# Performance work log

Measured on AMD Instinct MI355X. Metric: run time of the kernel, lower is better.

Reference implementation:

```python
import jax, jax.numpy as jnp
import numpy as np

B, S, H, E, V, T = 512, 140, 512, 256, 1000, 21  # T = day_walk_max + 1
PAD, SOS = 0, 2
NDAYS, DLEN = 7, 20


def setup_inputs() -> dict:
    key = jax.random.key(0)
    ks = jax.random.split(key, 16)
    s = 0.05
    return {
        "encoder_hidden": jax.random.normal(ks[0], (1, B, H), jnp.float32),
        "encoder_outputs": jax.random.normal(ks[1], (B, S, H), jnp.float32),
        "label": jax.random.randint(ks[2], (B, T + 1), 0, V),
        "numpairs": jax.random.randint(ks[3], (B, S), 0, 10),
        "emb": jax.random.normal(ks[4], (V, E), jnp.float32) * s,
        "W_ih": jax.random.normal(ks[5], (3 * H, E), jnp.float32) * s,
        "W_hh": jax.random.normal(ks[6], (3 * H, H), jnp.float32) * s,
        "b_ih": jnp.zeros((3 * H,), jnp.float32),
        "b_hh": jnp.zeros((3 * H,), jnp.float32),
        "attn_Wa": jax.random.normal(ks[7], (H, H), jnp.float32) * s,
        "wa_W": jax.random.normal(ks[8], (H, 2 * H), jnp.float32) * s,
        "fc_W": jax.random.normal(ks[9], (V, H), jnp.float32) * s,
        "fc_b": jnp.zeros((V,), jnp.float32),
    }


def _decode(encoder_hidden, encoder_outputs, label, numpairs,
            emb, W_ih, W_hh, b_ih, b_hh, attn_Wa, wa_W, fc_W, fc_b):
    # Luong 'general' attention over 7 day-segments of 20 steps each.
    enc_days = encoder_outputs.reshape(B, NDAYS, DLEN, H)
    mask_day = numpairs.reshape(B, NDAYS, DLEN) != PAD
    # energy is hidden-independent: precompute once  [B,7,20,H]
    energy_day = jnp.einsum('bdsh,gh->bdsg', enc_days, attn_Wa)

    def step(carry, lab_t):
        dec_in, h = carry  # dec_in [B] int, h [B,H]
        # per-day additive attention with numpair padding mask
        sc = jnp.einsum('bh,bdsh->bds', h, energy_day)
        sc = jnp.where(mask_day, sc, jnp.float32(-1e9))
        wd = jax.nn.softmax(sc, axis=-1)
        week = jnp.einsum('bds,bdsh->bdh', wd, enc_days)  # [B,7,H]
        # GRU cell (PyTorch gate layout r,z,n); dropout is identity at eval
        x = emb[dec_in]  # [B,E]
        gi = x @ W_ih.T + b_ih
        gh = h @ W_hh.T + b_hh
        i_r, i_z, i_n = jnp.split(gi, 3, axis=-1)
        h_r, h_z, h_n = jnp.split(gh, 3, axis=-1)
        r = jax.nn.sigmoid(i_r + h_r)
        z = jax.nn.sigmoid(i_z + h_z)
        n = jnp.tanh(i_n + r * h_n)
        h_new = (1.0 - z) * n + z * h  # [B,H]
        # week-level attention over the 7 day contexts (no mask)
        ew = jnp.einsum('bdh,gh->bdg', week, attn_Wa)
        aw = jax.nn.softmax(jnp.einsum('bh,bdh->bd', h_new, ew), axis=-1)
        ctx = jnp.einsum('bd,bdh->bh', aw, week)
        concat = jnp.concatenate([h_new, ctx], axis=-1)  # [B,2H]
        out = jax.nn.log_softmax(jnp.tanh(concat @ wa_W.T) @ fc_W.T + fc_b, axis=-1)
        return (lab_t, h_new), out  # teacher forcing: next input = label[:, t]

    dec0 = jnp.full((B,), SOS, dtype=label.dtype)
    h0 = encoder_hidden[0]  # [B,H]
    labels_t = label[:, :T].T  # [T,B]
    (last_in, _), outs = jax.lax.scan(step, (dec0, h0), labels_t)
    decoder_outputs = jnp.transpose(outs, (1, 0, 2))  # [B,T,V]
    return decoder_outputs, last_in[:, None]


def reference(encoder_hidden, encoder_outputs, label, numpairs,
              emb, W_ih, W_hh, b_ih, b_hh, attn_Wa, wa_W, fc_W, fc_b):
    return _decode(encoder_hidden, encoder_outputs, label, numpairs,
                   emb, W_ih, W_hh, b_ih, b_hh, attn_Wa, wa_W, fc_W, fc_b)
```

## Files before the change

### kernel.cpp

```cpp
#include <hip/hip_runtime.h>
#include <math.h>

typedef __attribute__((ext_vector_type(8))) short bf16x8;
typedef __attribute__((ext_vector_type(4))) float f32x4;

constexpr int NB = 512;
constexpr int NS = 140;
constexpr int NH = 512;
constexpr int NE = 256;
constexpr int NV = 1000;
constexpr int NVP = 1024;
constexpr int NT = 21;
constexpr int ND = 7;
constexpr int DL = 20;
constexpr int SOS = 2;
constexpr int LSTR = NT + 1;
constexpr int NROW = NT * NB;

__device__ __forceinline__ unsigned short f2bf(float f) {
  union { float f; unsigned u; } v; v.f = f;
  unsigned r = v.u + 0x7fffu + ((v.u >> 16) & 1u);
  return (unsigned short)(r >> 16);
}
__device__ __forceinline__ float bf2f(unsigned short h) {
  union { unsigned u; float f; } v; v.u = ((unsigned)h) << 16;
  return v.f;
}
__device__ __forceinline__ void unp8(uint4 v, float* o) {
  o[0] = bf2f((unsigned short)(v.x & 0xffffu)); o[1] = bf2f((unsigned short)(v.x >> 16));
  o[2] = bf2f((unsigned short)(v.y & 0xffffu)); o[3] = bf2f((unsigned short)(v.y >> 16));
  o[4] = bf2f((unsigned short)(v.z & 0xffffu)); o[5] = bf2f((unsigned short)(v.z >> 16));
  o[6] = bf2f((unsigned short)(v.w & 0xffffu)); o[7] = bf2f((unsigned short)(v.w >> 16));
}

template<int A16, int EPI, int OUT16>
__device__ __forceinline__ void gemm_body(
    const float* __restrict__ Af, const unsigned short* __restrict__ Ah,
    const unsigned short* __restrict__ Bt, const float* __restrict__ bias,
    float* __restrict__ C, unsigned short* __restrict__ C16,
    int K, int lda, int ldc, int bx, int by,
    unsigned short* As, unsigned short* Bs)
{
  const int tid = threadIdx.x;
  const int rowBase = by * 64, colBase = bx * 64;
  const int wave = tid >> 6, lane = tid & 63, quad = lane >> 4, l15 = lane & 15;
  const int rw = (wave & 1) * 32, cw = (wave >> 1) * 32;

  f32x4 acc[2][2];
#pragma unroll
  for (int i = 0; i < 2; ++i)
#pragma unroll
    for (int j = 0; j < 2; ++j)
#pragma unroll
      for (int r = 0; r < 4; ++r) acc[i][j][r] = 0.f;

  const int ar = tid >> 2;
  const int kq = (tid & 3) * 8;
  const float* aptrf = nullptr;
  const unsigned short* aptrh = nullptr;
  if (A16) aptrh = Ah + (size_t)(rowBase + ar) * lda + kq;
  else     aptrf = Af + (size_t)(rowBase + ar) * lda + kq;
  const unsigned short* bptr = Bt + (size_t)(colBase + ar) * K + kq;
  unsigned short* asd = &As[ar * 40 + kq];
  unsigned short* bsd = &Bs[ar * 40 + kq];

  float4 x0, x1;
  uint4 av;
  if (A16) {
    av = *(const uint4*)aptrh;
  } else {
    x0 = *(const float4*)aptrf; x1 = *(const float4*)(aptrf + 4);
  }
  uint4 bv = *(const uint4*)bptr;

  int cur = 0;
  for (int k0 = 0; k0 < K; k0 += 32) {
    uint4 aw;
    if (A16) {
      aw = av;
    } else {
      aw.x = (unsigned)f2bf(x0.x) | ((unsigned)f2bf(x0.y) << 16);
      aw.y = (unsigned)f2bf(x0.z) | ((unsigned)f2bf(x0.w) << 16);
      aw.z = (unsigned)f2bf(x1.x) | ((unsigned)f2bf(x1.y) << 16);
      aw.w = (unsigned)f2bf(x1.z) | ((unsigned)f2bf(x1.w) << 16);
    }
    *(uint4*)(asd + cur * 2560) = aw;
    *(uint4*)(bsd + cur * 2560) = bv;

    const int kn = k0 + 32;
    if (kn < K) {
      if (A16) {
        av = *(const uint4*)(aptrh + kn);
      } else {
        x0 = *(const float4*)(aptrf + kn);
        x1 = *(const float4*)(aptrf + kn + 4);
      }
      bv = *(const uint4*)(bptr + kn);
    }
    __syncthreads();

    const unsigned short* Ab = As + cur * 2560;
    const unsigned short* Bb = Bs + cur * 2560;
    const bf16x8 af0 = *(const bf16x8*)&Ab[(rw + l15) * 40 + quad * 8];
    const bf16x8 af1 = *(const bf16x8*)&Ab[(rw + 16 + l15) * 40 + quad * 8];
    const bf16x8 bf0 = *(const bf16x8*)&Bb[(cw + l15) * 40 + quad * 8];
    const bf16x8 bf1 = *(const bf16x8*)&Bb[(cw + 16 + l15) * 40 + quad * 8];
    acc[0][0] = __builtin_amdgcn_mfma_f32_16x16x32_bf16(af0, bf0, acc[0][0], 0, 0, 0);
    acc[0][1] = __builtin_amdgcn_mfma_f32_16x16x32_bf16(af0, bf1, acc[0][1], 0, 0, 0);
    acc[1][0] = __builtin_amdgcn_mfma_f32_16x16x32_bf16(af1, bf0, acc[1][0], 0, 0, 0);
    acc[1][1] = __builtin_amdgcn_mfma_f32_16x16x32_bf16(af1, bf1, acc[1][1], 0, 0, 0);
    cur ^= 1;
  }

#pragma unroll
  for (int i = 0; i < 2; ++i) {
    const int grow = rowBase + rw + 16 * i + quad * 4;
#pragma unroll
    for (int j = 0; j < 2; ++j) {
      const int gcol = colBase + cw + 16 * j + l15;
#pragma unroll
      for (int r = 0; r < 4; ++r) {
        float vo = acc[i][j][r];
        if (EPI == 1) vo += (gcol < NV) ? bias[gcol] : 0.f;
        if (EPI == 2) vo = tanhf(vo);
        if (OUT16) C16[(size_t)(grow + r) * ldc + gcol] = f2bf(vo);
        else       C[(size_t)(grow + r) * ldc + gcol] = vo;
      }
    }
  }
}

template<int A16, int EPI, int OUT16>
__global__ __launch_bounds__(256) void gemm_k(
    const float* __restrict__ Af, const unsigned short* __restrict__ Ah,
    const unsigned short* __restrict__ Bt, const float* __restrict__ bias,
    float* __restrict__ C, unsigned short* __restrict__ C16,
    int K, int lda, int ldc)
{
  __shared__ unsigned short As[2 * 64 * 40];
  __shared__ unsigned short Bs[2 * 64 * 40];
  gemm_body<A16, EPI, OUT16>(Af, Ah, Bt, bias, C, C16, K, lda, ldc,
                             blockIdx.x, blockIdx.y, As, Bs);
}

__global__ __launch_bounds__(256) void gemm_gather(
    const float* __restrict__ emb, const unsigned short* __restrict__ Wiht,
    unsigned short* __restrict__ Gi, const int* __restrict__ label)
{
  __shared__ unsigned short As[64 * 40];
  __shared__ unsigned short Bs[64 * 40];
  const int tid = threadIdx.x;
  const int rowBase = blockIdx.y * 64, colBase = blockIdx.x * 64;
  const int wave = tid >> 6, lane = tid & 63, quad = lane >> 4, l15 = lane & 15;
  const int rw = (wave & 1) * 32, cw = (wave >> 1) * 32;
  const int K = 256;

  f32x4 acc[2][2];
#pragma unroll
  for (int i = 0; i < 2; ++i)
#pragma unroll
    for (int j = 0; j < 2; ++j)
#pragma unroll
      for (int r = 0; r < 4; ++r) acc[i][j][r] = 0.f;

  const int ar = tid >> 2;
  const int kq = (tid & 3) * 8;
  const int aRowG = rowBase + ar;
  const int t = aRowG >> 9;
  const int b = aRowG & 511;
  const int dec = (t == 0) ? SOS : label[b * LSTR + (t - 1)];
  const float* aptr = emb + (size_t)dec * NE + kq;
  const unsigned short* bptr = Wiht + (size_t)(colBase + ar) * K + kq;
  unsigned short* asd = &As[ar * 40 + kq];
  unsigned short* bsd = &Bs[ar * 40 + kq];

  float4 x0 = *(const float4*)aptr;
  float4 x1 = *(const float4*)(aptr + 4);
  uint4 bv = *(const uint4*)bptr;

  for (int k0 = 0; k0 < K; k0 += 32) {
    uint4 aw;
    aw.x = (unsigned)f2bf(x0.x) | ((unsigned)f2bf(x0.y) << 16);
    aw.y = (unsigned)f2bf(x0.z) | ((unsigned)f2bf(x0.w) << 16);
    aw.z = (unsigned)f2bf(x1.x) | ((unsigned)f2bf(x1.y) << 16);
    aw.w = (unsigned)f2bf(x1.z) | ((unsigned)f2bf(x1.w) << 16);
    *(uint4*)asd = aw;
    *(uint4*)bsd = bv;
    __syncthreads();
    const int kn = k0 + 32;
    if (kn < K) {
      x0 = *(const float4*)(aptr + kn);
      x1 = *(const float4*)(aptr + kn + 4);
      bv = *(const uint4*)(bptr + kn);
    }
    const bf16x8 af0 = *(const bf16x8*)&As[(rw + l15) * 40 + quad * 8];
    const bf16x8 af1 = *(const bf16x8*)&As[(rw + 16 + l15) * 40 + quad * 8];
    const bf16x8 bf0 = *(const bf16x8*)&Bs[(cw + l15) * 40 + quad * 8];
    const bf16x8 bf1 = *(const bf16x8*)&Bs[(cw + 16 + l15) * 40 + quad * 8];
    acc[0][0] = __builtin_amdgcn_mfma_f32_16x16x32_bf16(af0, bf0, acc[0][0], 0, 0, 0);
    acc[0][1] = __builtin_amdgcn_mfma_f32_16x16x32_bf16(af0, bf1, acc[0][1], 0, 0, 0);
    acc[1][0] = __builtin_amdgcn_mfma_f32_16x16x32_bf16(af1, bf0, acc[1][0], 0, 0, 0);
    acc[1][1] = __builtin_amdgcn_mfma_f32_16x16x32_bf16(af1, bf1, acc[1][1], 0, 0, 0);
    __syncthreads();
  }

#pragma unroll
  for (int i = 0; i < 2; ++i) {
    const int grow = rowBase + rw + 16 * i + quad * 4;
#pragma unroll
    for (int j = 0; j < 2; ++j) {
      const int gcol = colBase + cw + 16 * j + l15;
#pragma unroll
      for (int r = 0; r < 4; ++r)
        Gi[(size_t)(grow + r) * 1536 + gcol] = f2bf(acc[i][j][r]);
    }
  }
}

__global__ __launch_bounds__(256) void step_fused(
    const float* __restrict__ Ht, const unsigned short* __restrict__ W1pk,
    const unsigned short* __restrict__ Gi_t,
    const float* __restrict__ b_ih, const float* __restrict__ b_hh,
    float* __restrict__ Hnext, float* __restrict__ Ut, int notLast)
{
  __shared__ __align__(16) char smem[46080];
  unsigned short* As = (unsigned short*)smem;
  unsigned short* Bs = (unsigned short*)(smem + 5120);
  float* Gbuf = (float*)smem;

  const int tid = threadIdx.x;
  const int wave = tid >> 6, lane = tid & 63, quad = lane >> 4, l15 = lane & 15;
  const int rowBase = blockIdx.y * 32;
  const int colBase = blockIdx.x * 256;

  f32x4 acc[2][4];
#pragma unroll
  for (int i = 0; i < 2; ++i)
#pragma unroll
    for (int j = 0; j < 4; ++j)
#pragma unroll
      for (int r = 0; r < 4; ++r) acc[i][j][r] = 0.f;

  const int ar = tid >> 3;
  const int kqa = (tid & 7) * 4;
  const float* aptr = Ht + (size_t)(rowBase + ar) * NH + kqa;
  const unsigned short* bbase = W1pk + (size_t)(colBase + tid) * 32;
  unsigned short* asd = As + ar * 40 + kqa;
  unsigned short* bsd = Bs + tid * 40;

  float4 xa = *(const float4*)aptr;
  uint4 bv0 = *(const uint4*)(bbase + 0);
  uint4 bv1 = *(const uint4*)(bbase + 8);
  uint4 bv2 = *(const uint4*)(bbase + 16);
  uint4 bv3 = *(const uint4*)(bbase + 24);

  int cur = 0;
  for (int k0 = 0; k0 < NH; k0 += 32) {
    ushort4 aw;
    aw.x = f2bf(xa.x); aw.y = f2bf(xa.y); aw.z = f2bf(xa.z); aw.w = f2bf(xa.w);
    *(ushort4*)(asd + cur * 1280) = aw;
    *(uint4*)(bsd + cur * 10240 + 0)  = bv0;
    *(uint4*)(bsd + cur * 10240 + 8)  = bv1;
    *(uint4*)(bsd + cur * 10240 + 16) = bv2;
    *(uint4*)(bsd + cur * 10240 + 24) = bv3;

    const int kn = k0 + 32;
    if (kn < NH) {
      xa = *(const float4*)(aptr + kn);
      const unsigned short* nb = bbase + (size_t)(kn >> 5) * (2048 * 32);
      bv0 = *(const uint4*)(nb + 0);
      bv1 = *(const uint4*)(nb + 8);
      bv2 = *(const uint4*)(nb + 16);
      bv3 = *(const uint4*)(nb + 24);
    }
    __syncthreads();

    const unsigned short* Ab = As + cur * 1280;
    const unsigned short* Bb = Bs + cur * 10240;
    const bf16x8 af0 = *(const bf16x8*)&Ab[(l15) * 40 + quad * 8];
    const bf16x8 af1 = *(const bf16x8*)&Ab[(16 + l15) * 40 + quad * 8];
#pragma unroll
    for (int j = 0; j < 4; ++j) {
      const bf16x8 bf = *(const bf16x8*)&Bb[(wave * 64 + j * 16 + l15) * 40 + quad * 8];
      acc[0][j] = __builtin_amdgcn_mfma_f32_16x16x32_bf16(af0, bf, acc[0][j], 0, 0, 0);
      acc[1][j] = __builtin_amdgcn_mfma_f32_16x16x32_bf16(af1, bf, acc[1][j], 0, 0, 0);
    }
    cur ^= 1;
  }
  __syncthreads();

#pragma unroll
  for (int i = 0; i < 2; ++i) {
#pragma unroll
    for (int j = 0; j < 4; ++j) {
#pragma unroll
      for (int r = 0; r < 4; ++r) {
        const int rl = 16 * i + quad * 4 + r;
        const int col = j * 16 + l15;
        if (wave == 3)
          Ut[(size_t)(rowBase + rl) * NH + blockIdx.x * 64 + col] = acc[i][j][r];
        else
          Gbuf[(wave * 32 + rl) * 72 + col] = acc[i][j][r];
      }
    }
  }
  __syncthreads();

  if (notLast) {
    const int rl = tid >> 3, c8 = (tid & 7) * 8;
    const int bg = rowBase + rl;
    const int jg = blockIdx.x * 64 + c8;
    const float* g0 = Gbuf + (0 * 32 + rl) * 72 + c8;
    const float* g1 = Gbuf + (1 * 32 + rl) * 72 + c8;
    const float* g2 = Gbuf + (2 * 32 + rl) * 72 + c8;
    const unsigned short* gp = Gi_t + (size_t)bg * 1536;
    float gr[8], gz[8], gn[8];
    { uint4 a = *(const uint4*)(gp + jg);        unp8(a, gr); }
    { uint4 a = *(const uint4*)(gp + 512 + jg);  unp8(a, gz); }
    { uint4 a = *(const uint4*)(gp + 1024 + jg); unp8(a, gn); }
    const float* hR = Ht + (size_t)bg * NH + jg;
    float* hW = Hnext + (size_t)bg * NH + jg;
    const float4 ho0 = *(const float4*)hR;
    const float4 ho1 = *(const float4*)(hR + 4);
    const float hov[8] = {ho0.x, ho0.y, ho0.z, ho0.w, ho1.x, ho1.y, ho1.z, ho1.w};
    float o[8];
#pragma unroll
    for (int c = 0; c < 8; ++c) {
      const int j = jg + c;
      const float ir  = gr[c] + b_ih[j];
      const float iz  = gz[c] + b_ih[512 + j];
      const float inn = gn[c] + b_ih[1024 + j];
      const float hr  = g0[c] + b_hh[j];
      const float hz  = g1[c] + b_hh[512 + j];
      const float hn  = g2[c] + b_hh[1024 + j];
      const float rg = 1.f / (1.f + expf(-(ir + hr)));
      const float zg = 1.f / (1.f + expf(-(iz + hz)));
      const float ng = tanhf(inn + rg * hn);
      o[c] = (1.f - zg) * ng + zg * hov[c];
    }
    *(float4*)hW = make_float4(o[0], o[1], o[2], o[3]);
    *(float4*)(hW + 4) = make_float4(o[4], o[5], o[6], o[7]);
  }
}

__global__ __launch_bounds__(256) void day_attn_mfma(
    const float* __restrict__ enc, const int* __restrict__ numpairs,
    const float* __restrict__ U, unsigned short* __restrict__ week)
{
  __shared__ unsigned short Erow[32 * 520];
  __shared__ unsigned short ETs[512 * 40];
  __shared__ float S_lds[32 * 33];
  __shared__ unsigned short P_lds[32 * 40];

  const int tid = threadIdx.x;
  const int wave = tid >> 6, lane = tid & 63;
  const int quad = lane >> 4, l15 = lane & 15;
  const int b = blockIdx.x / ND, d = blockIdx.x % ND;
  const int mt = wave >> 1, nt = wave & 1;

  {
    unsigned* p2 = (unsigned*)ETs;
    for (int i = tid; i < 10240; i += 256) p2[i] = 0;
    unsigned* p3 = (unsigned*)P_lds;
    for (int i = tid; i < 640; i += 256) p3[i] = 0;
  }

  const float* eb = enc + ((size_t)b * NS + d * DL) * NH;
  for (int f = tid; f < DL * NH / 4; f += 256) {
    const int s = f >> 7, c4 = f & 127, h = c4 * 4;
    const float4 v = *(const float4*)(eb + s * NH + h);
    const unsigned short h0 = f2bf(v.x), h1 = f2bf(v.y),
                         h2 = f2bf(v.z), h3 = f2bf(v.w);
    ushort4 hs; hs.x = h0; hs.y = h1; hs.z = h2; hs.w = h3;
    *(ushort4*)&Erow[s * 520 + h] = hs;
    ETs[(h + 0) * 40 + s] = h0;
    ETs[(h + 1) * 40 + s] = h1;
    ETs[(h + 2) * 40 + s] = h2;
    ETs[(h + 3) * 40 + s] = h3;
  }

  bf16x8 qa[16];
  {
    const int m = mt * 16 + l15;
    const int t = (m < NT + 1) ? m : NT;
    const float* qp = U + ((size_t)t * NB + b) * NH + quad * 8;
#pragma unroll
    for (int ks = 0; ks < 16; ++ks) {
      const float4 lo = *(const float4*)(qp + ks * 32);
      const float4 hi = *(const float4*)(qp + ks * 32 + 4);
      union { bf16x8 v; ushort u[8]; } pk;
      pk.u[0] = f2bf(lo.x); pk.u[1] = f2bf(lo.y); pk.u[2] = f2bf(lo.z); pk.u[3] = f2bf(lo.w);
      pk.u[4] = f2bf(hi.x); pk.u[5] = f2bf(hi.y); pk.u[6] = f2bf(hi.z); pk.u[7] = f2bf(hi.w);
      qa[ks] = pk.v;
    }
  }
  __syncthreads();

  f32x4 sacc = {0.f, 0.f, 0.f, 0.f};
#pragma unroll
  for (int ks = 0; ks < 16; ++ks) {
    const bf16x8 bf = *(const bf16x8*)&Erow[(nt * 16 + l15) * 520 + ks * 32 + quad * 8];
    sacc = __builtin_amdgcn_mfma_f32_16x16x32_bf16(qa[ks], bf, sacc, 0, 0, 0);
  }
#pragma unroll
  for (int r = 0; r < 4; ++r)
    S_lds[(mt * 16 + quad * 4 + r) * 33 + nt * 16 + l15] = sacc[r];
  __syncthreads();

  {
    const int r = tid >> 3, c = tid & 7;
    const int base = b * NS + d * DL;
    float v0 = S_lds[r * 33 + c];
    if (numpairs[base + c] == 0) v0 = -1e9f;
    float v1 = S_lds[r * 33 + c + 8];
    if (numpairs[base + c + 8] == 0) v1 = -1e9f;
    float v2 = -1e30f;
    if (c < 4) {
      v2 = S_lds[r * 33 + c + 16];
      if (numpairs[base + c + 16] == 0) v2 = -1e9f;
    }
    float mx = fmaxf(fmaxf(v0, v1), v2);
    mx = fmaxf(mx, __shfl_xor(mx, 1));
    mx = fmaxf(mx, __shfl_xor(mx, 2));
    mx = fmaxf(mx, __shfl_xor(mx, 4));
    const float e0 = expf(v0 - mx), e1 = expf(v1 - mx);
    const float e2 = (c < 4) ? expf(v2 - mx) : 0.f;
    float sm = e0 + e1 + e2;
    sm += __shfl_xor(sm, 1);
    sm += __shfl_xor(sm, 2);
    sm += __shfl_xor(sm, 4);
    const float inv = 1.f / sm;
    P_lds[r * 40 + c] = f2bf(e0 * inv);
    P_lds[r * 40 + c + 8] = f2bf(e1 * inv);
    if (c < 4) P_lds[r * 40 + c + 16] = f2bf(e2 * inv);
  }
  __syncthreads();

  const bf16x8 pa = *(const bf16x8*)&P_lds[(mt * 16 + l15) * 40 + quad * 8];
#pragma unroll
  for (int j = 0; j < 16; ++j) {
    const int hcol = nt * 256 + j * 16;
    const bf16x8 bf = *(const bf16x8*)&ETs[(hcol + l15) * 40 + quad * 8];
    f32x4 oacc = {0.f, 0.f, 0.f, 0.f};
    oacc = __builtin_amdgcn_mfma_f32_16x16x32_bf16(pa, bf, oacc, 0, 0, 0);
#pragma unroll
    for (int r = 0; r < 4; ++r) {
      const int t = mt * 16 + quad * 4 + r;
      if (t < NT)
        week[(((size_t)t * NB + b) * ND + d) * NH + hcol + l15] = f2bf(oacc[r]);
    }
  }
}

__global__ __launch_bounds__(256) void wk_ctx(
    const float* __restrict__ U, const unsigned short* __restrict__ week,
    const float* __restrict__ H, unsigned short* __restrict__ concat)
{
  __shared__ float scS[16 * ND];
  __shared__ float awS[16 * ND];
  const int tid = threadIdx.x;
  const int t = blockIdx.x >> 5;
  const int grp = blockIdx.x & 31;
  const int b16 = tid >> 4, k16 = tid & 15;
  const int b = grp * 16 + b16;
  const float* vp = U + ((size_t)(t + 1) * NB + b) * NH + k16 * 32;
  const size_t wrow = ((size_t)t * NB + b) * ND;

  for (int d = 0; d < ND; ++d) {
    const unsigned short* wp = week + (wrow + d) * NH + k16 * 32;
    float p = 0.f;
#pragma unroll
    for (int q = 0; q < 8; ++q) {
      const float4 a = *(const float4*)(vp + q * 4);
      const ushort4 wv = *(const ushort4*)(wp + q * 4);
      p += a.x * bf2f(wv.x) + a.y * bf2f(wv.y) + a.z * bf2f(wv.z) + a.w * bf2f(wv.w);
    }
    p += __shfl_down(p, 8); p += __shfl_down(p, 4);
    p += __shfl_down(p, 2); p += __shfl_down(p, 1);
    if (k16 == 0) scS[b16 * ND + d] = p;
  }
  __syncthreads();
  if (tid < 16) {
    float s[ND], mx = -1e30f;
    for (int d = 0; d < ND; ++d) { s[d] = scS[tid * ND + d]; mx = fmaxf(mx, s[d]); }
    float sum = 0.f;
    for (int d = 0; d < ND; ++d) { float e = expf(s[d] - mx); s[d] = e; sum += e; }
    const float inv = 1.f / sum;
    for (int d = 0; d < ND; ++d) awS[tid * ND + d] = s[d] * inv;
  }
  __syncthreads();

  const int c0 = k16 * 32;
  const float* hp = H + ((size_t)(t + 1) * NB + b) * NH + c0;
  float aw[ND];
#pragma unroll
  for (int d = 0; d < ND; ++d) aw[d] = awS[b16 * ND + d];
  unsigned short* crow = concat + ((size_t)t * NB + b) * 1024;
#pragma unroll
  for (int q = 0; q < 8; ++q) {
    const int c = c0 + q * 4;
    const float4 hv = *(const float4*)(hp + q * 4);
    ushort4 hs;
    hs.x = f2bf(hv.x); hs.y = f2bf(hv.y); hs.z = f2bf(hv.z); hs.w = f2bf(hv.w);
    *(ushort4*)(crow + c) = hs;
    float4 cv = make_float4(0.f, 0.f, 0.f, 0.f);
#pragma unroll
    for (int d = 0; d < ND; ++d) {
      const ushort4 wv = *(const ushort4*)(week + (wrow + d) * NH + c);
      cv.x += aw[d] * bf2f(wv.x); cv.y += aw[d] * bf2f(wv.y);
      cv.z += aw[d] * bf2f(wv.z); cv.w += aw[d] * bf2f(wv.w);
    }
    ushort4 cs;
    cs.x = f2bf(cv.x); cs.y = f2bf(cv.y); cs.z = f2bf(cv.z); cs.w = f2bf(cv.w);
    *(ushort4*)(crow + 512 + c) = cs;
  }
}

__global__ __launch_bounds__(256) void lsm_k(
    const float* __restrict__ logits, float* __restrict__ out)
{
  __shared__ float red[8];
  const int tid = threadIdx.x;
  const int wave = tid >> 6, lane = tid & 63;
  const int r = blockIdx.x;
  const int t = r >> 9, b = r & (NB - 1);
  const float* row = logits + (size_t)r * NVP;
  float v[4];
  float mx = -1e30f;
#pragma unroll
  for (int k = 0; k < 4; ++k) {
    const int c = tid + k * 256;
    v[k] = row[c];
    if (c < NV) mx = fmaxf(mx, v[k]);
  }
#pragma unroll
  for (int off = 32; off; off >>= 1) mx = fmaxf(mx, __shfl_xor(mx, off));
  if (lane == 0) red[wave] = mx;
  __syncthreads();
  mx = fmaxf(fmaxf(red[0], red[1]), fmaxf(red[2], red[3]));
  float s = 0.f;
#pragma unroll
  for (int k = 0; k < 4; ++k) {
    const int c = tid + k * 256;
    if (c < NV) s += expf(v[k] - mx);
  }
#pragma unroll
  for (int off = 32; off; off >>= 1) s += __shfl_xor(s, off);
  if (lane == 0) red[4 + wave] = s;
  __syncthreads();
  const float lse = mx + logf(red[4] + red[5] + red[6] + red[7]);
  float* orow = out + ((size_t)b * NT + t) * NV;
#pragma unroll
  for (int k = 0; k < 4; ++k) {
    const int c = tid + k * 256;
    if (c < NV) orow[c] = v[k] - lse;
  }
}

__global__ void write_last(const int* __restrict__ label, float* __restrict__ out2)
{
  const int b = blockIdx.x * 256 + threadIdx.x;
  if (b < NB) out2[b] = (float)label[b * LSTR + (NT - 1)];
}

__global__ __launch_bounds__(256) void pack_w1pk(
    const float* __restrict__ Whh, const float* __restrict__ Wa,
    unsigned short* __restrict__ W1pk)
{
  const int idx = blockIdx.x * 256 + threadIdx.x;
  const int np = idx >> 9, k = idx & 511;
  const int g = np >> 8, rem = np & 255, gate = rem >> 6, j = g * 64 + (rem & 63);
  float v;
  if (gate < 3) v = Whh[(size_t)(gate * 512 + j) * 512 + k];
  else          v = Wa[(size_t)k * 512 + j];
  W1pk[((size_t)(k >> 5) * 2048 + np) * 32 + (k & 31)] = f2bf(v);
}

__global__ __launch_bounds__(256) void cast4(
    const float4* __restrict__ in, ushort4* __restrict__ out, int n4)
{
  const int i = blockIdx.x * 256 + threadIdx.x;
  if (i < n4) {
    const float4 x = in[i];
    ushort4 r;
    r.x = f2bf(x.x); r.y = f2bf(x.y); r.z = f2bf(x.z); r.w = f2bf(x.w);
    out[i] = r;
  }
}

extern "C" void kernel_launch(void* const* d_in, const int* in_sizes, int n_in,
                              void* d_out, int out_size, void* d_ws, size_t ws_size,
                              hipStream_t stream)
{
  const float* enc_h  = (const float*)d_in[0];
  const float* enc    = (const float*)d_in[1];
  const int*   label  = (const int*)d_in[2];
  const int*   numprs = (const int*)d_in[3];
  const float* emb    = (const float*)d_in[4];
  const float* W_ih   = (const float*)d_in[5];
  const float* W_hh   = (const float*)d_in[6];
  const float* b_ih   = (const float*)d_in[7];
  const float* b_hh   = (const float*)d_in[8];
  const float* Wa     = (const float*)d_in[9];
  const float* wa_W   = (const float*)d_in[10];
  const float* fc_W   = (const float*)d_in[11];
  const float* fc_b   = (const float*)d_in[12];
  float* out = (float*)d_out;

  float* f = (float*)d_ws;
  float* H_all   = f; f += (size_t)(NT + 1) * NB * NH;
  float* U_all   = f; f += (size_t)(NT + 1) * NB * NH;
  float* logitsW = f; f += (size_t)NROW * NVP;
  unsigned short* us = (unsigned short*)f;
  unsigned short* W1pk   = us; us += (size_t)2048 * 512;
  unsigned short* W3t    = us; us += (size_t)512 * 1024;
  unsigned short* W4t    = us; us += (size_t)NVP * 512;
  unsigned short* Wiht   = us; us += (size_t)1536 * 256;
  unsigned short* Gi     = us; us += (size_t)NT * NB * 1536;
  unsigned short* week   = us; us += (size_t)NT * NB * ND * NH;
  unsigned short* concatW= us; us += (size_t)NROW * 1024;
  unsigned short* aBuf   = us; us += (size_t)NROW * 512;

  const dim3 blk(256);
  const size_t BH = (size_t)NB * NH;

  hipMemcpyAsync(H_all, enc_h, BH * sizeof(float),
                 hipMemcpyDeviceToDevice, stream);

  pack_w1pk<<<dim3(2048 * 512 / 256), blk, 0, stream>>>(W_hh, Wa, W1pk);
  cast4<<<dim3(512 * 1024 / 4 / 256), blk, 0, stream>>>(
      (const float4*)wa_W, (ushort4*)W3t, 512 * 1024 / 4);
  cast4<<<dim3((NV * 512 / 4 + 255) / 256), blk, 0, stream>>>(
      (const float4*)fc_W, (ushort4*)W4t, NV * 512 / 4);
  hipMemsetAsync(W4t + (size_t)NV * 512, 0, (size_t)(NVP - NV) * 512 * 2, stream);
  cast4<<<dim3(1536 * 256 / 4 / 256), blk, 0, stream>>>(
      (const float4*)W_ih, (ushort4*)Wiht, 1536 * 256 / 4);
  gemm_gather<<<dim3(24, NT * 8), blk, 0, stream>>>(emb, Wiht, Gi, label);

  for (int t = 0; t <= NT; ++t) {
    const int notLast = (t < NT) ? 1 : 0;
    const int tg = (t < NT) ? t : NT - 1;
    step_fused<<<dim3(8, 16), blk, 0, stream>>>(
        H_all + (size_t)t * BH, W1pk, Gi + (size_t)tg * NB * 1536,
        b_ih, b_hh,
        H_all + (size_t)(notLast ? t + 1 : t) * BH,
        U_all + (size_t)t * BH, notLast);
  }

  day_attn_mfma<<<dim3(NB * ND), blk, 0, stream>>>(enc, numprs, U_all, week);
  wk_ctx<<<dim3(NT * 32), blk, 0, stream>>>(U_all, week, H_all, concatW);
  gemm_k<1, 2, 1><<<dim3(8, NROW / 64), blk, 0, stream>>>(
      nullptr, concatW, W3t, nullptr, nullptr, aBuf, 1024, 1024, 512);
  gemm_k<1, 1, 0><<<dim3(16, NROW / 64), blk, 0, stream>>>(
      nullptr, aBuf, W4t, fc_b, logitsW, nullptr, 512, 512, NVP);
  lsm_k<<<dim3(NROW), blk, 0, stream>>>(logitsW, out);
  write_last<<<dim3(2), blk, 0, stream>>>(label, out + (size_t)NB * NT * NV);
}
```

Baseline: 792.1 us.

## Run GRU recurrence as one cooperative persistent kernel and store U in bf16

Replaces the 22 per-step GRU kernel launches with a single cooperative kernel of 128 blocks that loops over time steps and uses grid.sync between steps, removing per-launch overhead and tail gaps. The K chunk grows from 32 to 64 (with W1pk repacked to match) so there are fewer LDS syncs per step. The attention projection U is written as bf16 instead of fp32, which halves its traffic and lets day_attn and wk_ctx load it without conversion. day_attn now builds its transposed encoder tile from LDS with a narrower stride and only zeroes the padding. The risks are grid-sync cost, the larger shared-memory footprint limiting co-residency, and the last step reading Gi at t=0 (its result is unused because notLast is 0).

```diff
diff --git a/kernel.cpp b/kernel.cpp
--- a/kernel.cpp
+++ b/kernel.cpp
@@ -1,5 +1,8 @@
 #include <hip/hip_runtime.h>
+#include <hip/hip_cooperative_groups.h>
 #include <math.h>
+
+namespace cg = cooperative_groups;
 
 typedef __attribute__((ext_vector_type(8))) short bf16x8;
 typedef __attribute__((ext_vector_type(4))) float f32x4;
@@ -217,138 +220,154 @@
   }
 }
 
-__global__ __launch_bounds__(256) void step_fused(
-    const float* __restrict__ Ht, const unsigned short* __restrict__ W1pk,
-    const unsigned short* __restrict__ Gi_t,
+__global__ __launch_bounds__(256) void gru_all(
+    float* __restrict__ H_all, const unsigned short* __restrict__ W1pk,
+    const unsigned short* __restrict__ Gi,
     const float* __restrict__ b_ih, const float* __restrict__ b_hh,
-    float* __restrict__ Hnext, float* __restrict__ Ut, int notLast)
-{
-  __shared__ __align__(16) char smem[46080];
+    unsigned short* __restrict__ U16)
+{
+  __shared__ __align__(16) char smem[82944];
   unsigned short* As = (unsigned short*)smem;
-  unsigned short* Bs = (unsigned short*)(smem + 5120);
+  unsigned short* Bs = (unsigned short*)(smem + 9216);
   float* Gbuf = (float*)smem;
 
   const int tid = threadIdx.x;
   const int wave = tid >> 6, lane = tid & 63, quad = lane >> 4, l15 = lane & 15;
   const int rowBase = blockIdx.y * 32;
   const int colBase = blockIdx.x * 256;
-
-  f32x4 acc[2][4];
-#pragma unroll
-  for (int i = 0; i < 2; ++i)
-#pragma unroll
-    for (int j = 0; j < 4; ++j)
-#pragma unroll
-      for (int r = 0; r < 4; ++r) acc[i][j][r] = 0.f;
-
-  const int ar = tid >> 3;
-  const int kqa = (tid & 7) * 4;
-  const float* aptr = Ht + (size_t)(rowBase + ar) * NH + kqa;
-  const unsigned short* bbase = W1pk + (size_t)(colBase + tid) * 32;
-  unsigned short* asd = As + ar * 40 + kqa;
-  unsigned short* bsd = Bs + tid * 40;
-
-  float4 xa = *(const float4*)aptr;
-  uint4 bv0 = *(const uint4*)(bbase + 0);
-  uint4 bv1 = *(const uint4*)(bbase + 8);
-  uint4 bv2 = *(const uint4*)(bbase + 16);
-  uint4 bv3 = *(const uint4*)(bbase + 24);
-
-  int cur = 0;
-  for (int k0 = 0; k0 < NH; k0 += 32) {
-    ushort4 aw;
-    aw.x = f2bf(xa.x); aw.y = f2bf(xa.y); aw.z = f2bf(xa.z); aw.w = f2bf(xa.w);
-    *(ushort4*)(asd + cur * 1280) = aw;
-    *(uint4*)(bsd + cur * 10240 + 0)  = bv0;
-    *(uint4*)(bsd + cur * 10240 + 8)  = bv1;
-    *(uint4*)(bsd + cur * 10240 + 16) = bv2;
-    *(uint4*)(bsd + cur * 10240 + 24) = bv3;
-
-    const int kn = k0 + 32;
-    if (kn < NH) {
-      xa = *(const float4*)(aptr + kn);
-      const unsigned short* nb = bbase + (size_t)(kn >> 5) * (2048 * 32);
-      bv0 = *(const uint4*)(nb + 0);
-      bv1 = *(const uint4*)(nb + 8);
-      bv2 = *(const uint4*)(nb + 16);
-      bv3 = *(const uint4*)(nb + 24);
+  const int arow = tid >> 3;
+  const int akq  = (tid & 7) * 8;
+  const size_t BH = (size_t)NB * NH;
+  cg::grid_group grid = cg::this_grid();
+
+  for (int t = 0; t <= NT; ++t) {
+    const float* Ht = H_all + (size_t)t * BH;
+    float* Hn = H_all + (size_t)(t + 1) * BH;
+    const unsigned short* Gt = Gi + (size_t)((t < NT) ? t : 0) * NB * 1536;
+    unsigned short* Ut = U16 + (size_t)t * BH;
+    const int notLast = (t < NT) ? 1 : 0;
+
+    f32x4 acc[2][4];
+#pragma unroll
+    for (int i = 0; i < 2; ++i)
+#pragma unroll
+      for (int j = 0; j < 4; ++j)
+#pragma unroll
+        for (int r = 0; r < 4; ++r) acc[i][j][r] = 0.f;
+
+    const float* aptr = Ht + (size_t)(rowBase + arow) * NH + akq;
+    const unsigned short* bptr = W1pk + ((size_t)colBase + tid) * 64;
+
+    float4 xa0 = *(const float4*)aptr;
+    float4 xa1 = *(const float4*)(aptr + 4);
+    uint4 bv[8];
+#pragma unroll
+    for (int q = 0; q < 8; ++q) bv[q] = ((const uint4*)bptr)[q];
+
+    int cur = 0;
+    for (int c = 0; c < 8; ++c) {
+      uint4 aw;
+      aw.x = (unsigned)f2bf(xa0.x) | ((unsigned)f2bf(xa0.y) << 16);
+      aw.y = (unsigned)f2bf(xa0.z) | ((unsigned)f2bf(xa0.w) << 16);
+      aw.z = (unsigned)f2bf(xa1.x) | ((unsigned)f2bf(xa1.y) << 16);
+      aw.w = (unsigned)f2bf(xa1.z) | ((unsigned)f2bf(xa1.w) << 16);
+      *(uint4*)&As[((cur << 5) + arow) * 72 + akq] = aw;
+      {
+        unsigned short* bd = &Bs[((cur << 8) + tid) * 72];
+#pragma unroll
+        for (int q = 0; q < 8; ++q) ((uint4*)bd)[q] = bv[q];
+      }
+      const int cn = c + 1;
+      if (cn < 8) {
+        const float* ap = aptr + cn * 64;
+        xa0 = *(const float4*)ap;
+        xa1 = *(const float4*)(ap + 4);
+        const unsigned short* bp = bptr + (size_t)cn * (2048 * 64);
+#pragma unroll
+        for (int q = 0; q < 8; ++q) bv[q] = ((const uint4*)bp)[q];
+      }
+      __syncthreads();
+
+      const unsigned short* Ab = As + (cur << 5) * 72;
+      const unsigned short* Bb = Bs + (cur << 8) * 72;
+#pragma unroll
+      for (int kk = 0; kk < 2; ++kk) {
+        const bf16x8 af0 = *(const bf16x8*)&Ab[(l15) * 72 + kk * 32 + quad * 8];
+        const bf16x8 af1 = *(const bf16x8*)&Ab[(16 + l15) * 72 + kk * 32 + quad * 8];
+#pragma unroll
+        for (int j = 0; j < 4; ++j) {
+          const bf16x8 bf = *(const bf16x8*)&Bb[(wave * 64 + j * 16 + l15) * 72 + kk * 32 + quad * 8];
+          acc[0][j] = __builtin_amdgcn_mfma_f32_16x16x32_bf16(af0, bf, acc[0][j], 0, 0, 0);
+          acc[1][j] = __builtin_amdgcn_mfma_f32_16x16x32_bf16(af1, bf, acc[1][j], 0, 0, 0);
+        }
+      }
+      cur ^= 1;
     }
     __syncthreads();
 
-    const unsigned short* Ab = As + cur * 1280;
-    const unsigned short* Bb = Bs + cur * 10240;
-    const bf16x8 af0 = *(const bf16x8*)&Ab[(l15) * 40 + quad * 8];
-    const bf16x8 af1 = *(const bf16x8*)&Ab[(16 + l15) * 40 + quad * 8];
-#pragma unroll
-    for (int j = 0; j < 4; ++j) {
-      const bf16x8 bf = *(const bf16x8*)&Bb[(wave * 64 + j * 16 + l15) * 40 + quad * 8];
-      acc[0][j] = __builtin_amdgcn_mfma_f32_16x16x32_bf16(af0, bf, acc[0][j], 0, 0, 0);
-      acc[1][j] = __builtin_amdgcn_mfma_f32_16x16x32_bf16(af1, bf, acc[1][j], 0, 0, 0);
-    }
-    cur ^= 1;
-  }
-  __syncthreads();
-
-#pragma unroll
-  for (int i = 0; i < 2; ++i) {
-#pragma unroll
-    for (int j = 0; j < 4; ++j) {
-#pragma unroll
-      for (int r = 0; r < 4; ++r) {
-        const int rl = 16 * i + quad * 4 + r;
-        const int col = j * 16 + l15;
-        if (wave == 3)
-          Ut[(size_t)(rowBase + rl) * NH + blockIdx.x * 64 + col] = acc[i][j][r];
-        else
-          Gbuf[(wave * 32 + rl) * 72 + col] = acc[i][j][r];
+#pragma unroll
+    for (int i = 0; i < 2; ++i) {
+#pragma unroll
+      for (int j = 0; j < 4; ++j) {
+#pragma unroll
+        for (int r = 0; r < 4; ++r) {
+          const int rl = 16 * i + quad * 4 + r;
+          const int col = j * 16 + l15;
+          if (wave == 3)
+            Ut[(size_t)(rowBase + rl) * NH + blockIdx.x * 64 + col] = f2bf(acc[i][j][r]);
+          else
+            Gbuf[(wave * 32 + rl) * 72 + col] = acc[i][j][r];
+        }
       }
     }
-  }
-  __syncthreads();
-
-  if (notLast) {
-    const int rl = tid >> 3, c8 = (tid & 7) * 8;
-    const int bg = rowBase + rl;
-    const int jg = blockIdx.x * 64 + c8;
-    const float* g0 = Gbuf + (0 * 32 + rl) * 72 + c8;
-    const float* g1 = Gbuf + (1 * 32 + rl) * 72 + c8;
-    const float* g2 = Gbuf + (2 * 32 + rl) * 72 + c8;
-    const unsigned short* gp = Gi_t + (size_t)bg * 1536;
-    float gr[8], gz[8], gn[8];
-    { uint4 a = *(const uint4*)(gp + jg);        unp8(a, gr); }
-    { uint4 a = *(const uint4*)(gp + 512 + jg);  unp8(a, gz); }
-    { uint4 a = *(const uint4*)(gp + 1024 + jg); unp8(a, gn); }
-    const float* hR = Ht + (size_t)bg * NH + jg;
-    float* hW = Hnext + (size_t)bg * NH + jg;
-    const float4 ho0 = *(const float4*)hR;
-    const float4 ho1 = *(const float4*)(hR + 4);
-    const float hov[8] = {ho0.x, ho0.y, ho0.z, ho0.w, ho1.x, ho1.y, ho1.z, ho1.w};
-    float o[8];
-#pragma unroll
-    for (int c = 0; c < 8; ++c) {
-      const int j = jg + c;
-      const float ir  = gr[c] + b_ih[j];
-      const float iz  = gz[c] + b_ih[512 + j];
-      const float inn = gn[c] + b_ih[1024 + j];
-      const float hr  = g0[c] + b_hh[j];
-      const float hz  = g1[c] + b_hh[512 + j];
-      const float hn  = g2[c] + b_hh[1024 + j];
-      const float rg = 1.f / (1.f + expf(-(ir + hr)));
-      const float zg = 1.f / (1.f + expf(-(iz + hz)));
-      const float ng = tanhf(inn + rg * hn);
-      o[c] = (1.f - zg) * ng + zg * hov[c];
-    }
-    *(float4*)hW = make_float4(o[0], o[1], o[2], o[3]);
-    *(float4*)(hW + 4) = make_float4(o[4], o[5], o[6], o[7]);
+    __syncthreads();
+
+    if (notLast) {
+      const int rl = tid >> 3, c8 = (tid & 7) * 8;
+      const int bg = rowBase + rl;
+      const int jg = blockIdx.x * 64 + c8;
+      const float* g0 = Gbuf + (0 * 32 + rl) * 72 + c8;
+      const float* g1 = Gbuf + (1 * 32 + rl) * 72 + c8;
+      const float* g2 = Gbuf + (2 * 32 + rl) * 72 + c8;
+      const unsigned short* gp = Gt + (size_t)bg * 1536;
+      float gr[8], gz[8], gn[8];
+      { uint4 a = *(const uint4*)(gp + jg);        unp8(a, gr); }
+      { uint4 a = *(const uint4*)(gp + 512 + jg);  unp8(a, gz); }
+      { uint4 a = *(const uint4*)(gp + 1024 + jg); unp8(a, gn); }
+      const float* hR = Ht + (size_t)bg * NH + jg;
+      float* hW = Hn + (size_t)bg * NH + jg;
+      const float4 ho0 = *(const float4*)hR;
+      const float4 ho1 = *(const float4*)(hR + 4);
+      const float hov[8] = {ho0.x, ho0.y, ho0.z, ho0.w, ho1.x, ho1.y, ho1.z, ho1.w};
+      float o[8];
+#pragma unroll
+      for (int c = 0; c < 8; ++c) {
+        const int j = jg + c;
+        const float ir  = gr[c] + b_ih[j];
+        const float iz  = gz[c] + b_ih[512 + j];
+        const float inn = gn[c] + b_ih[1024 + j];
+        const float hr  = g0[c] + b_hh[j];
+        const float hz  = g1[c] + b_hh[512 + j];
+        const float hn  = g2[c] + b_hh[1024 + j];
+        const float rg = 1.f / (1.f + expf(-(ir + hr)));
+        const float zg = 1.f / (1.f + expf(-(iz + hz)));
+        const float ng = tanhf(inn + rg * hn);
+        o[c] = (1.f - zg) * ng + zg * hov[c];
+      }
+      *(float4*)hW = make_float4(o[0], o[1], o[2], o[3]);
+      *(float4*)(hW + 4) = make_float4(o[4], o[5], o[6], o[7]);
+    }
+    __threadfence();
+    grid.sync();
   }
 }
 
 __global__ __launch_bounds__(256) void day_attn_mfma(
     const float* __restrict__ enc, const int* __restrict__ numpairs,
-    const float* __restrict__ U, unsigned short* __restrict__ week)
+    const unsigned short* __restrict__ U16, unsigned short* __restrict__ week)
 {
   __shared__ unsigned short Erow[32 * 520];
-  __shared__ unsigned short ETs[512 * 40];
+  __shared__ unsigned short ETs[512 * 36];
   __shared__ float S_lds[32 * 33];
   __shared__ unsigned short P_lds[32 * 40];
 
@@ -358,43 +377,38 @@
   const int b = blockIdx.x / ND, d = blockIdx.x % ND;
   const int mt = wave >> 1, nt = wave & 1;
 
-  {
-    unsigned* p2 = (unsigned*)ETs;
-    for (int i = tid; i < 10240; i += 256) p2[i] = 0;
-    unsigned* p3 = (unsigned*)P_lds;
-    for (int i = tid; i < 640; i += 256) p3[i] = 0;
-  }
+  for (int i = tid; i < 512 * 6; i += 256)
+    *(unsigned*)&ETs[(i / 6) * 36 + 20 + (i % 6) * 2] = 0;
+  for (int i = tid; i < 640; i += 256) ((unsigned*)P_lds)[i] = 0;
 
   const float* eb = enc + ((size_t)b * NS + d * DL) * NH;
   for (int f = tid; f < DL * NH / 4; f += 256) {
-    const int s = f >> 7, c4 = f & 127, h = c4 * 4;
+    const int s = f >> 7, h = (f & 127) * 4;
     const float4 v = *(const float4*)(eb + s * NH + h);
-    const unsigned short h0 = f2bf(v.x), h1 = f2bf(v.y),
-                         h2 = f2bf(v.z), h3 = f2bf(v.w);
-    ushort4 hs; hs.x = h0; hs.y = h1; hs.z = h2; hs.w = h3;
+    ushort4 hs;
+    hs.x = f2bf(v.x); hs.y = f2bf(v.y); hs.z = f2bf(v.z); hs.w = f2bf(v.w);
     *(ushort4*)&Erow[s * 520 + h] = hs;
-    ETs[(h + 0) * 40 + s] = h0;
-    ETs[(h + 1) * 40 + s] = h1;
-    ETs[(h + 2) * 40 + s] = h2;
-    ETs[(h + 3) * 40 + s] = h3;
   }
 
   bf16x8 qa[16];
   {
     const int m = mt * 16 + l15;
     const int t = (m < NT + 1) ? m : NT;
-    const float* qp = U + ((size_t)t * NB + b) * NH + quad * 8;
-#pragma unroll
-    for (int ks = 0; ks < 16; ++ks) {
-      const float4 lo = *(const float4*)(qp + ks * 32);
-      const float4 hi = *(const float4*)(qp + ks * 32 + 4);
-      union { bf16x8 v; ushort u[8]; } pk;
-      pk.u[0] = f2bf(lo.x); pk.u[1] = f2bf(lo.y); pk.u[2] = f2bf(lo.z); pk.u[3] = f2bf(lo.w);
-      pk.u[4] = f2bf(hi.x); pk.u[5] = f2bf(hi.y); pk.u[6] = f2bf(hi.z); pk.u[7] = f2bf(hi.w);
-      qa[ks] = pk.v;
-    }
+    const unsigned short* qp = U16 + ((size_t)t * NB + b) * NH + quad * 8;
+#pragma unroll
+    for (int ks = 0; ks < 16; ++ks)
+      qa[ks] = *(const bf16x8*)(qp + ks * 32);
   }
   __syncthreads();
+
+  for (int i = tid; i < 64 * DL; i += 256) {
+    const int s = i % DL, h8 = i / DL;
+    const uint4 v = *(const uint4*)&Erow[s * 520 + h8 * 8];
+    const unsigned short* u = (const unsigned short*)&v;
+#pragma unroll
+    for (int c = 0; c < 8; ++c)
+      ETs[(h8 * 8 + c) * 36 + s] = u[c];
+  }
 
   f32x4 sacc = {0.f, 0.f, 0.f, 0.f};
 #pragma unroll
@@ -440,7 +454,7 @@
 #pragma unroll
   for (int j = 0; j < 16; ++j) {
     const int hcol = nt * 256 + j * 16;
-    const bf16x8 bf = *(const bf16x8*)&ETs[(hcol + l15) * 40 + quad * 8];
+    const bf16x8 bf = *(const bf16x8*)&ETs[(hcol + l15) * 36 + quad * 8];
     f32x4 oacc = {0.f, 0.f, 0.f, 0.f};
     oacc = __builtin_amdgcn_mfma_f32_16x16x32_bf16(pa, bf, oacc, 0, 0, 0);
 #pragma unroll
@@ -453,7 +467,7 @@
 }
 
 __global__ __launch_bounds__(256) void wk_ctx(
-    const float* __restrict__ U, const unsigned short* __restrict__ week,
+    const unsigned short* __restrict__ U16, const unsigned short* __restrict__ week,
     const float* __restrict__ H, unsigned short* __restrict__ concat)
 {
   __shared__ float scS[16 * ND];
@@ -463,17 +477,26 @@
   const int grp = blockIdx.x & 31;
   const int b16 = tid >> 4, k16 = tid & 15;
   const int b = grp * 16 + b16;
-  const float* vp = U + ((size_t)(t + 1) * NB + b) * NH + k16 * 32;
+  const unsigned short* vp = U16 + ((size_t)(t + 1) * NB + b) * NH + k16 * 32;
   const size_t wrow = ((size_t)t * NB + b) * ND;
+
+  float va[32];
+#pragma unroll
+  for (int q = 0; q < 4; ++q) {
+    const uint4 av = ((const uint4*)vp)[q];
+    unp8(av, va + q * 8);
+  }
 
   for (int d = 0; d < ND; ++d) {
     const unsigned short* wp = week + (wrow + d) * NH + k16 * 32;
     float p = 0.f;
 #pragma unroll
-    for (int q = 0; q < 8; ++q) {
-      const float4 a = *(const float4*)(vp + q * 4);
-      const ushort4 wv = *(const ushort4*)(wp + q * 4);
-      p += a.x * bf2f(wv.x) + a.y * bf2f(wv.y) + a.z * bf2f(wv.z) + a.w * bf2f(wv.w);
+    for (int q = 0; q < 4; ++q) {
+      const uint4 wv = ((const uint4*)wp)[q];
+      float w8[8];
+      unp8(wv, w8);
+#pragma unroll
+      for (int c = 0; c < 8; ++c) p += va[q * 8 + c] * w8[c];
     }
     p += __shfl_down(p, 8); p += __shfl_down(p, 4);
     p += __shfl_down(p, 2); p += __shfl_down(p, 1);
@@ -573,7 +596,7 @@
   float v;
   if (gate < 3) v = Whh[(size_t)(gate * 512 + j) * 512 + k];
   else          v = Wa[(size_t)k * 512 + j];
-  W1pk[((size_t)(k >> 5) * 2048 + np) * 32 + (k & 31)] = f2bf(v);
+  W1pk[((size_t)(k >> 6) * 2048 + np) * 64 + (k & 63)] = f2bf(v);
 }
 
 __global__ __launch_bounds__(256) void cast4(
@@ -609,9 +632,9 @@
 
   float* f = (float*)d_ws;
   float* H_all   = f; f += (size_t)(NT + 1) * NB * NH;
-  float* U_all   = f; f += (size_t)(NT + 1) * NB * NH;
   float* logitsW = f; f += (size_t)NROW * NVP;
   unsigned short* us = (unsigned short*)f;
+  unsigned short* U16    = us; us += (size_t)(NT + 1) * NB * NH;
   unsigned short* W1pk   = us; us += (size_t)2048 * 512;
   unsigned short* W3t    = us; us += (size_t)512 * 1024;
   unsigned short* W4t    = us; us += (size_t)NVP * 512;
@@ -637,18 +660,13 @@
       (const float4*)W_ih, (ushort4*)Wiht, 1536 * 256 / 4);
   gemm_gather<<<dim3(24, NT * 8), blk, 0, stream>>>(emb, Wiht, Gi, label);
 
-  for (int t = 0; t <= NT; ++t) {
-    const int notLast = (t < NT) ? 1 : 0;
-    const int tg = (t < NT) ? t : NT - 1;
-    step_fused<<<dim3(8, 16), blk, 0, stream>>>(
-        H_all + (size_t)t * BH, W1pk, Gi + (size_t)tg * NB * 1536,
-        b_ih, b_hh,
-        H_all + (size_t)(notLast ? t + 1 : t) * BH,
-        U_all + (size_t)t * BH, notLast);
-  }
-
-  day_attn_mfma<<<dim3(NB * ND), blk, 0, stream>>>(enc, numprs, U_all, week);
-  wk_ctx<<<dim3(NT * 32), blk, 0, stream>>>(U_all, week, H_all, concatW);
+  {
+    void* args[] = {&H_all, &W1pk, &Gi, (void*)&b_ih, (void*)&b_hh, &U16};
+    hipLaunchCooperativeKernel((void*)gru_all, dim3(8, 16), blk, args, 0, stream);
+  }
+
+  day_attn_mfma<<<dim3(NB * ND), blk, 0, stream>>>(enc, numprs, U16, week);
+  wk_ctx<<<dim3(NT * 32), blk, 0, stream>>>(U16, week, H_all, concatW);
   gemm_k<1, 2, 1><<<dim3(8, NROW / 64), blk, 0, stream>>>(
       nullptr, concatW, W3t, nullptr, nullptr, aBuf, 1024, 1024, 512);
   gemm_k<1, 1, 0><<<dim3(16, NROW / 64), blk, 0, stream>>>(
```

After: 1.823 ms. +130.1%, slower.
